# Kernel tuning notes

Measured on AMD Instinct MI355X. Metric: run time of the kernel, lower is better.

The kernel has to match this reference:

```python
import jax, jax.numpy as jnp
import numpy as np

H, HS, C = 16, 64, 1024  # num_heads, head_size, n_embd

def setup_inputs() -> dict:
    key = jax.random.key(0)
    ks = jax.random.split(key, 5)
    B, T = 2, 2048
    s = 1.0 / np.sqrt(C)
    return {
        "x": jax.random.normal(ks[0], (B, T, C), dtype=jnp.float32),
        "Wq": jax.random.normal(ks[1], (H, C, HS), dtype=jnp.float32) * s,
        "Wk": jax.random.normal(ks[2], (H, C, HS), dtype=jnp.float32) * s,
        "Wv": jax.random.normal(ks[3], (H, C, HS), dtype=jnp.float32) * s,
        "Wo": jax.random.normal(ks[4], (C, C), dtype=jnp.float32) * s,
    }

def reference(x, Wq, Wk, Wv, Wo):
    B, T, Cdim = x.shape
    scale = Cdim ** -0.5  # original scales by n_embd**-0.5, not head_size
    q = jnp.einsum('btc,hcd->bhtd', x, Wq)
    k = jnp.einsum('btc,hcd->bhtd', x, Wk)
    v = jnp.einsum('btc,hcd->bhtd', x, Wv)
    wei = jnp.einsum('bhtd,bhsd->bhts', q, k) * scale  # [B,H,T,T]
    causal = jnp.tril(jnp.ones((T, T), dtype=bool))
    wei = jnp.where(causal, wei, -jnp.inf)
    wei = jax.nn.softmax(wei, axis=-1)
    out = jnp.einsum('bhts,bhsd->bhtd', wei, v)  # [B,H,T,HS]
    out = out.transpose(0, 2, 1, 3).reshape(B, T, -1)  # concat heads -> [B,T,C]
    return out @ Wo.T
```

## Files before the change

kernel.cpp:

```cpp
#include <hip/hip_runtime.h>

typedef unsigned short ushort_t;
typedef __bf16 bf16x8 __attribute__((ext_vector_type(8)));
typedef float f32x4 __attribute__((ext_vector_type(4)));
typedef float f32x16 __attribute__((ext_vector_type(16)));
typedef unsigned short ushortx8 __attribute__((ext_vector_type(8)));
typedef unsigned int uintx4 __attribute__((ext_vector_type(4)));

#define NH 16
#define HS 64
#define CD 1024
#define NB 2
#define NT 2048
#define BT (NB * NT)
#define N3 (3 * CD)

#define L2E_DIV32 0.04508422002778011f

#define QKV_LD 2048
#define SLOT_BYTES 18432
#define WAVE_BYTES 4608
#define R0_SLOTS 796

__constant__ static const int QB_TAB[51] = {
  0,1,2, 3,3, 4,4, 5,5, 6,6,6, 7,7,7, 8,8,8,
  9,9,9,9, 10,10,10,10, 11,11,11,11,
  12,12,12,12,12, 13,13,13,13,13, 14,14,14,14,14,
  15,15,15,15,15,15};
__constant__ static const int K_TAB[51] = {
  1,1,1, 2,2, 2,2, 2,2, 3,3,3, 3,3,3, 3,3,3,
  4,4,4,4, 4,4,4,4, 4,4,4,4,
  5,5,5,5,5, 5,5,5,5,5, 5,5,5,5,5,
  6,6,6,6,6,6};
__constant__ static const int T0_TAB[51] = {
  0, 0, 0, 0,4, 0,5, 0,6, 0,5,10, 0,6,11, 0,6,12,
  0,5,10,15, 0,6,12,17, 0,6,12,18,
  0,6,11,16,21, 0,6,12,18,23, 0,6,12,18,24,
  0,6,12,17,22,27};
__constant__ static const int T1_TAB[51] = {
  2, 4, 6, 4,8, 5,10, 6,12, 5,10,14, 6,11,16, 6,12,18,
  5,10,15,20, 6,12,17,22, 6,12,18,24,
  6,11,16,21,26, 6,12,18,23,28, 6,12,18,24,30,
  6,12,17,22,27,32};
__constant__ static const int FIRSTC_TAB[16] = {
  0,1,2,3,5,7,9,12,15,18,22,26,30,35,40,45};


__device__ __forceinline__ ushort_t bf16_rne(float f) {
  union { float f; unsigned u; } v; v.f = f;
  unsigned u = v.u;
  unsigned r = (u + 0x7FFFu + ((u >> 16) & 1u)) >> 16;
  return (ushort_t)r;
}

__device__ __forceinline__ float bf2f(ushort_t u) {
  union { unsigned u; float f; } v; v.u = ((unsigned)u) << 16; return v.f;
}

__device__ __forceinline__ void gload_lds16(const ushort_t* g, ushort_t* l) {
  __builtin_amdgcn_global_load_lds(
      (const __attribute__((address_space(1))) unsigned int*)g,
      (__attribute__((address_space(3))) unsigned int*)l, 16, 0, 0);
}

__device__ __forceinline__ f32x4 mfma16(ushortx8 a, ushortx8 b, f32x4 c) {
  return __builtin_amdgcn_mfma_f32_16x16x32_bf16(
      __builtin_bit_cast(bf16x8, a), __builtin_bit_cast(bf16x8, b), c, 0, 0, 0);
}

__device__ __forceinline__ f32x16 mfma32(ushortx8 a, ushortx8 b, f32x16 c) {
  return __builtin_amdgcn_mfma_f32_32x32x16_bf16(
      __builtin_bit_cast(bf16x8, a), __builtin_bit_cast(bf16x8, b), c, 0, 0, 0);
}

__device__ __forceinline__ unsigned cvt_pk_bf16(float lo, float hi) {
  unsigned r;
  asm("v_cvt_pk_bf16_f32 %0, %1, %2" : "=v"(r) : "v"(lo), "v"(hi));
  return r;
}

__device__ __forceinline__ void plswap(unsigned &a, unsigned &b) {
  asm volatile("v_permlane32_swap_b32 %0, %1" : "+v"(a), "+v"(b));
}

__device__ __forceinline__ const char* slot_ptr(const char* wsb, const char* dout, int s) {
  return (s < R0_SLOTS) ? wsb + (size_t)s * SLOT_BYTES
                        : dout + (size_t)(s - R0_SLOTS) * SLOT_BYTES;
}


__global__ __launch_bounds__(256)
void pack_cast(const float4* __restrict__ in, ushort_t* __restrict__ out, int n4) {
  const int i = blockIdx.x * 256 + threadIdx.x;
  if (i >= n4) return;
  const float4 v = in[i];
  ushort4 r;
  r.x = bf16_rne(v.x); r.y = bf16_rne(v.y);
  r.z = bf16_rne(v.z); r.w = bf16_rne(v.w);
  *(ushort4*)(out + (size_t)i * 4) = r;
}

__global__ __launch_bounds__(256)
void pack_wqkv(const float* __restrict__ Wq, const float* __restrict__ Wk,
               const float* __restrict__ Wv, ushort_t* __restrict__ out) {
  __shared__ ushort_t tile[64 * 66];
  const int sh = blockIdx.y;
  const int s = sh >> 4, h = sh & 15;
  const float* W = (s == 0) ? Wq : ((s == 1) ? Wk : Wv);
  const int c0 = blockIdx.x * 64;
  const int t = threadIdx.x;
#pragma unroll
  for (int j = 0; j < 16; ++j) {
    const int idx = t + j * 256;
    const int ci = idx >> 6, d = idx & 63;
    const float v = W[(size_t)(h * 1024 + c0 + ci) * 64 + d];
    tile[d * 66 + ci] = bf16_rne(v);
  }
  __syncthreads();
#pragma unroll
  for (int j = 0; j < 16; ++j) {
    const int idx = t + j * 256;
    const int d = idx >> 6, ci = idx & 63;
    out[(size_t)(s * 1024 + h * 64 + d) * 1024 + c0 + ci] = tile[d * 66 + ci];
  }
}


template <int MODE>
__global__ __launch_bounds__(256)
void gemm_bt(const ushort_t* __restrict__ A, const ushort_t* __restrict__ Bt,
             void* __restrict__ Cv, ushort_t* __restrict__ Vt,
             int M, int N, int K) {
  __shared__ __align__(16) ushort_t ldsA[2][128 * 32];
  __shared__ __align__(16) ushort_t ldsB[2][128 * 32];
  const int tid = threadIdx.x;
  const int lane = tid & 63;
  const int wave = tid >> 6;
  const int row0 = blockIdx.y * 128;
  const int col0 = blockIdx.x * 128;
  const int wm = wave >> 1, wn = wave & 1;

  f32x4 acc[4][4] = {};

  const int ce = (tid & 3) * 8;

  auto stage = [&](int buf, int kt) {
    const int kbase = kt * 32;
#pragma unroll
    for (int j = 0; j < 2; ++j) {
      const int r = j * 64 + (tid >> 2);
      gload_lds16(A + (size_t)(row0 + r) * K + kbase + ce,
                  &ldsA[buf][(j * 256 + wave * 64) * 8]);
      gload_lds16(Bt + (size_t)(col0 + r) * K + kbase + ce,
                  &ldsB[buf][(j * 256 + wave * 64) * 8]);
    }
  };

  const int arow_off = (wm * 64 + (lane & 15)) * 32 + (lane >> 4) * 8;
  const int brow_off = (wn * 64 + (lane & 15)) * 32 + (lane >> 4) * 8;

  auto compute = [&](int buf) {
    ushortx8 af[4], bfr[4];
#pragma unroll
    for (int m = 0; m < 4; ++m)
      af[m] = *(const ushortx8*)&ldsA[buf][arow_off + m * 512];
#pragma unroll
    for (int n = 0; n < 4; ++n)
      bfr[n] = *(const ushortx8*)&ldsB[buf][brow_off + n * 512];
#pragma unroll
    for (int m = 0; m < 4; ++m)
#pragma unroll
      for (int n = 0; n < 4; ++n)
        acc[m][n] = mfma16(af[m], bfr[n], acc[m][n]);
  };

  stage(0, 0);
  __syncthreads();
  const int nk = K >> 5;
  for (int kt = 0; kt < nk; ++kt) {
    const int cur = kt & 1;
    if (kt + 1 < nk) stage(cur ^ 1, kt + 1);
    compute(cur);
    __syncthreads();
  }

#pragma unroll
  for (int m = 0; m < 4; ++m) {
    const int rbase = row0 + wm * 64 + m * 16 + (lane >> 4) * 4;
#pragma unroll
    for (int n = 0; n < 4; ++n) {
      const int col = col0 + wn * 64 + n * 16 + (lane & 15);
      if constexpr (MODE == 0) {
#pragma unroll
        for (int i = 0; i < 4; ++i)
          ((float*)Cv)[(size_t)(rbase + i) * N + col] = acc[m][n][i];
      } else {
        if (col < 2048) {
          const float sc = (col < 1024) ? L2E_DIV32 : 1.0f;
#pragma unroll
          for (int i = 0; i < 4; ++i)
            ((ushort_t*)Cv)[(size_t)(rbase + i) * QKV_LD + col] =
                bf16_rne(acc[m][n][i] * sc);
        } else {
          const int dcol = col - 2048;
          const int bI = rbase >> 11;
          const int t0i = rbase & 2047;
          ushort4 pk;
          pk.x = bf16_rne(acc[m][n][0]);
          pk.y = bf16_rne(acc[m][n][1]);
          pk.z = bf16_rne(acc[m][n][2]);
          pk.w = bf16_rne(acc[m][n][3]);
          *(ushort4*)(Vt + (size_t)(bI * 1024 + dcol) * NT + t0i) = pk;
        }
      }
    }
  }
}


__global__ __launch_bounds__(256, 4)
void attn_fwd9(const ushort_t* __restrict__ QKV, const ushort_t* __restrict__ Vt,
               ushort_t* __restrict__ O, char* __restrict__ wsb,
               char* __restrict__ dout) {
  __shared__ __align__(16) ushort_t KV[2][2][4096];

  const int tid = threadIdx.x;
  const int lane = tid & 63;
  const int w = tid >> 6;
  const int l31 = lane & 31;
  const int h = lane >> 5;

  const int x = blockIdx.x;
  const int bh = x & 31;
  const int c = 50 - (x >> 5);
  const int qb = QB_TAB[c];
  const int k  = K_TAB[c];
  const int t0 = T0_TAB[c];
  const int t1 = T1_TAB[c];
  const int nt = 2 * qb + 2;
  const bool lastc = (t1 == nt);

  const int b = bh >> 4, head = bh & 15;
  const size_t base = (size_t)b * NT * QKV_LD;
  const int qg = qb * 128 + w * 32 + l31;
  const int tmax = lastc ? (2 * qb + (w >> 1)) : (t1 - 1);

  int koff[4];
#pragma unroll
  for (int kc = 0; kc < 4; ++kc)
    koff[kc] = l31 * 128 + (((2 * kc + h) ^ (l31 & 7)) * 16);

  const int rowA = tid >> 3, ccA = tid & 7;
  const int rowB = 32 + rowA;
  const ushort_t* kg = QKV + base + 1024 + head * 64;
  const ushort_t* vg = Vt + (size_t)(bh * 64) * NT;
  const ushort_t* ksA = kg + (size_t)(t0 * 64 + rowA) * QKV_LD + ((ccA ^ (rowA & 7)) * 8);
  const ushort_t* ksB = kg + (size_t)(t0 * 64 + rowB) * QKV_LD + ((ccA ^ (rowB & 7)) * 8);
  const ushort_t* vsA = vg + (size_t)rowA * NT + t0 * 64 + ((ccA ^ (rowA & 7)) * 8);
  const ushort_t* vsB = vg + (size_t)rowB * NT + t0 * 64 + ((ccA ^ (rowB & 7)) * 8);
  const size_t kadv = (size_t)64 * QKV_LD;

  gload_lds16(ksA, &KV[0][0][w * 512]);
  gload_lds16(ksB, &KV[0][0][2048 + w * 512]);
  gload_lds16(vsA, &KV[0][1][w * 512]);
  gload_lds16(vsB, &KV[0][1][2048 + w * 512]);

  ushortx8 qf[4];
  {
    const ushort_t* qp = QKV + base + (size_t)qg * QKV_LD + head * 64 + h * 8;
#pragma unroll
    for (int kc = 0; kc < 4; ++kc) qf[kc] = *(const ushortx8*)(qp + kc * 16);
  }

  f32x16 oA = {}, oB = {};
  float m_r = -INFINITY, l_r = 0.f;

  auto half_pass = [&](f32x16 s, const char* vb, const int kc0, const bool msk) {
    if (msk) {
#pragma unroll
      for (int r = 0; r < 16; ++r) {
        const int krow = (r & 3) + 8 * (r >> 2) + 4 * h;
        if (krow > l31) s[r] = -INFINITY;
      }
    }
    float mm[8];
#pragma unroll
    for (int r = 0; r < 8; ++r) mm[r] = fmaxf(s[r], s[r + 8]);
#pragma unroll
    for (int st = 4; st >= 1; st >>= 1)
#pragma unroll
      for (int r = 0; r < st; ++r) mm[r] = fmaxf(mm[r], mm[r + st]);
    const float mx = fmaxf(mm[0], __shfl_xor(mm[0], 32, 64));
    if (__any(mx > m_r + 8.0f)) {
      const float mn = fmaxf(m_r, mx);
      const float al = exp2f(m_r - mn);
      m_r = mn; l_r *= al;
#pragma unroll
      for (int r = 0; r < 16; ++r) { oA[r] *= al; oB[r] *= al; }
    }
    unsigned u[8];
    float ps[4];
#pragma unroll
    for (int jj = 0; jj < 4; ++jj) ps[jj] = 0.f;
#pragma unroll
    for (int jj = 0; jj < 8; ++jj) {
      const float e0 = exp2f(s[2 * jj] - m_r);
      const float e1 = exp2f(s[2 * jj + 1] - m_r);
      u[jj] = cvt_pk_bf16(e0, e1);
      ps[jj & 3] += e0 + e1;
    }
    ps[0] += ps[2]; ps[1] += ps[3]; ps[0] += ps[1];
    l_r += ps[0] + __shfl_xor(ps[0], 32, 64);
    plswap(u[0], u[2]); plswap(u[1], u[3]);
    plswap(u[4], u[6]); plswap(u[5], u[7]);
#pragma unroll
    for (int q2 = 0; q2 < 2; ++q2) {
      uintx4 pw;
      pw[0] = u[4 * q2 + 0]; pw[1] = u[4 * q2 + 1];
      pw[2] = u[4 * q2 + 2]; pw[3] = u[4 * q2 + 3];
      const ushortx8 pav = __builtin_bit_cast(ushortx8, pw);
      oA = mfma32(*(const ushortx8*)(vb + koff[kc0 + q2]), pav, oA);
      oB = mfma32(*(const ushortx8*)(vb + 4096 + koff[kc0 + q2]), pav, oB);
    }
  };

  int curb = 0;
  for (int t = t0; t < t1; ++t) {
    const int nxt = curb ^ 1;
    if (t + 1 < t1) {
      ksA += kadv; ksB += kadv; vsA += 64; vsB += 64;
      gload_lds16(ksA, &KV[nxt][0][w * 512]);
      gload_lds16(ksB, &KV[nxt][0][2048 + w * 512]);
      gload_lds16(vsA, &KV[nxt][1][w * 512]);
      gload_lds16(vsB, &KV[nxt][1][2048 + w * 512]);
      asm volatile("s_waitcnt vmcnt(4)" ::: "memory");
    } else {
      asm volatile("s_waitcnt vmcnt(0)" ::: "memory");
    }
    __builtin_amdgcn_s_barrier();
    asm volatile("" ::: "memory");

    if (t <= tmax) {
      const bool diag = lastc && (t == tmax);
      const bool halfB = diag && ((w & 1) == 0);
      const char* kb = (const char*)&KV[curb][0][0];
      const char* vb = (const char*)&KV[curb][1][0];

      {
        f32x16 sA = {};
#pragma unroll
        for (int kc = 0; kc < 4; ++kc)
          sA = mfma32(*(const ushortx8*)(kb + koff[kc]), qf[kc], sA);
        half_pass(sA, vb, 0, diag && halfB);
      }
      if (!halfB) {
        f32x16 sB = {};
#pragma unroll
        for (int kc = 0; kc < 4; ++kc)
          sB = mfma32(*(const ushortx8*)(kb + 4096 + koff[kc]), qf[kc], sB);
        half_pass(sB, vb, 2, diag);
      }
    }

    __builtin_amdgcn_s_barrier();
    asm volatile("" ::: "memory");
    curb ^= 1;
  }

  if (k == 1) {
    const float inv_l = 1.0f / l_r;
    ushort_t* op = O + ((size_t)(b * NT + qg)) * 1024 + head * 64;
#pragma unroll
    for (int db = 0; db < 2; ++db)
#pragma unroll
      for (int g = 0; g < 4; ++g) {
        ushort4 pk;
        pk.x = bf16_rne((db ? oB[4 * g + 0] : oA[4 * g + 0]) * inv_l);
        pk.y = bf16_rne((db ? oB[4 * g + 1] : oA[4 * g + 1]) * inv_l);
        pk.z = bf16_rne((db ? oB[4 * g + 2] : oA[4 * g + 2]) * inv_l);
        pk.w = bf16_rne((db ? oB[4 * g + 3] : oA[4 * g + 3]) * inv_l);
        *(ushort4*)(op + db * 32 + 8 * g + 4 * h) = pk;
      }
  } else {
    const int s = bh * 51 + c;
    char* wb = (char*)slot_ptr(wsb, dout, s) + w * WAVE_BYTES;
#pragma unroll
    for (int g = 0; g < 4; ++g) {
      ushortx8 pk;
#pragma unroll
      for (int e2 = 0; e2 < 8; ++e2)
        pk[e2] = bf16_rne(g < 2 ? oA[g * 8 + e2] : oB[(g - 2) * 8 + e2]);
      *(ushortx8*)(wb + lane * 64 + g * 16) = pk;
    }
    *(float*)(wb + 4096 + lane * 4) = m_r;
    *(float*)(wb + 4352 + lane * 4) = l_r;
  }
}

__global__ __launch_bounds__(256)
void attn_merge(const char* __restrict__ wsb, const char* __restrict__ dout,
                ushort_t* __restrict__ O) {
  const int x = blockIdx.x;
  const int bh = x & 31;
  const int qb = 3 + (x >> 5);
  const int f = FIRSTC_TAB[qb];
  const int k = K_TAB[f];
  const int tid = threadIdx.x;
  const int lane = tid & 63;
  const int w = tid >> 6;
  const int l31 = lane & 31;
  const int h = lane >> 5;
  const int sbase = bh * 51 + f;

  float M = -INFINITY;
  for (int jj = 0; jj < k; ++jj) {
    const char* wb = slot_ptr(wsb, dout, sbase + jj) + w * WAVE_BYTES;
    M = fmaxf(M, *(const float*)(wb + 4096 + lane * 4));
  }
  float o[32];
#pragma unroll
  for (int r = 0; r < 32; ++r) o[r] = 0.f;
  float lacc = 0.f;
  for (int jj = 0; jj < k; ++jj) {
    const char* wb = slot_ptr(wsb, dout, sbase + jj) + w * WAVE_BYTES;
    const float a = exp2f(*(const float*)(wb + 4096 + lane * 4) - M);
    lacc += a * *(const float*)(wb + 4352 + lane * 4);
#pragma unroll
    for (int g = 0; g < 4; ++g) {
      const ushortx8 v = *(const ushortx8*)(wb + lane * 64 + g * 16);
#pragma unroll
      for (int e = 0; e < 8; ++e) o[g * 8 + e] += a * bf2f(v[e]);
    }
  }
  const float inv_l = 1.0f / lacc;
  const int b = bh >> 4, head = bh & 15;
  const int qg = qb * 128 + w * 32 + l31;
  ushort_t* op = O + ((size_t)(b * NT + qg)) * 1024 + head * 64;
#pragma unroll
  for (int db = 0; db < 2; ++db)
#pragma unroll
    for (int g = 0; g < 4; ++g) {
      ushort4 pk;
      pk.x = bf16_rne(o[db * 16 + 4 * g + 0] * inv_l);
      pk.y = bf16_rne(o[db * 16 + 4 * g + 1] * inv_l);
      pk.z = bf16_rne(o[db * 16 + 4 * g + 2] * inv_l);
      pk.w = bf16_rne(o[db * 16 + 4 * g + 3] * inv_l);
      *(ushort4*)(op + db * 32 + 8 * g + 4 * h) = pk;
    }
}


extern "C" void kernel_launch(void* const* d_in, const int* in_sizes, int n_in,
                              void* d_out, int out_size, void* d_ws, size_t ws_size,
                              hipStream_t stream) {
  (void)in_sizes; (void)n_in; (void)out_size; (void)ws_size;
  const float* x  = (const float*)d_in[0];
  const float* Wq = (const float*)d_in[1];
  const float* Wk = (const float*)d_in[2];
  const float* Wv = (const float*)d_in[3];
  const float* Wo = (const float*)d_in[4];

  char* ws = (char*)d_ws;
  ushort_t* Xbf    = (ushort_t*)(ws);
  ushort_t* Wqkv_t = (ushort_t*)(ws + 8388608);
  ushort_t* Wo_bf  = (ushort_t*)(ws + 14680064);
  ushort_t* QKV    = (ushort_t*)(ws + 16777216);
  ushort_t* Vt     = (ushort_t*)(ws + 33554432);
  ushort_t* Obf    = (ushort_t*)(ws + 41943040);

  pack_cast<<<4096, 256, 0, stream>>>((const float4*)x, Xbf, 1048576);
  pack_cast<<<1024, 256, 0, stream>>>((const float4*)Wo, Wo_bf, 262144);
  pack_wqkv<<<dim3(16, 48), 256, 0, stream>>>(Wq, Wk, Wv, Wqkv_t);

  gemm_bt<1><<<dim3(24, 32), 256, 0, stream>>>(Xbf, Wqkv_t, QKV, Vt, BT, N3, CD);
  attn_fwd9<<<1632, 256, 0, stream>>>(QKV, Vt, Obf, ws, (char*)d_out);
  attn_merge<<<416, 256, 0, stream>>>(ws, (char*)d_out, Obf);
  gemm_bt<0><<<dim3(8, 32), 256, 0, stream>>>(Obf, Wo_bf, d_out, nullptr, BT, CD, CD);
}
```

Before: 131.0 us.

## Repartition causal attention into 32 chunks per head and fuse cast kernels

Replaces the 51-chunk split-KV schedule per batch-head with a 32-chunk schedule. Each query block is split into 1-3 chunks of roughly equal KV-tile count, so the attention grid drops from 1632 to 1024 blocks and the merge grid from 416 to 352. A new lookup table maps each merged query block to its partial slots. It also fuses the two fp32-to-bf16 cast launches into one. The intent is to cut per-block overhead and the number of partial results to merge, at the risk of worse tail balance across CUs.

```diff
diff --git a/kernel.cpp b/kernel.cpp
--- a/kernel.cpp
+++ b/kernel.cpp
@@ -22,28 +22,21 @@
 #define WAVE_BYTES 4608
 #define R0_SLOTS 796
 
-__constant__ static const int QB_TAB[51] = {
-  0,1,2, 3,3, 4,4, 5,5, 6,6,6, 7,7,7, 8,8,8,
-  9,9,9,9, 10,10,10,10, 11,11,11,11,
-  12,12,12,12,12, 13,13,13,13,13, 14,14,14,14,14,
-  15,15,15,15,15,15};
-__constant__ static const int K_TAB[51] = {
-  1,1,1, 2,2, 2,2, 2,2, 3,3,3, 3,3,3, 3,3,3,
-  4,4,4,4, 4,4,4,4, 4,4,4,4,
-  5,5,5,5,5, 5,5,5,5,5, 5,5,5,5,5,
-  6,6,6,6,6,6};
-__constant__ static const int T0_TAB[51] = {
-  0, 0, 0, 0,4, 0,5, 0,6, 0,5,10, 0,6,11, 0,6,12,
-  0,5,10,15, 0,6,12,17, 0,6,12,18,
-  0,6,11,16,21, 0,6,12,18,23, 0,6,12,18,24,
-  0,6,12,17,22,27};
-__constant__ static const int T1_TAB[51] = {
-  2, 4, 6, 4,8, 5,10, 6,12, 5,10,14, 6,11,16, 6,12,18,
-  5,10,15,20, 6,12,17,22, 6,12,18,24,
-  6,11,16,21,26, 6,12,18,23,28, 6,12,18,24,30,
-  6,12,17,22,27,32};
-__constant__ static const int FIRSTC_TAB[16] = {
-  0,1,2,3,5,7,9,12,15,18,22,26,30,35,40,45};
+__constant__ static const int QB_TAB[32] = {
+  10,10,15,15, 4, 9, 9,13,14,14,14,15, 8, 8,12,12,
+  13,13, 3, 7, 7,11,11,11,12, 6, 6, 2, 5, 5, 1, 0};
+__constant__ static const int T0_TAB[32] = {
+   0,11, 0,11, 0, 0,10, 0, 0,10,20,22, 0, 9, 0, 9,
+  10,19, 0, 0, 8, 0, 8,16,18, 0, 7, 0, 0, 6, 0, 0};
+__constant__ static const int T1_TAB[32] = {
+  11,22,11,22,10,10,20,10,10,20,30,32, 9,18, 9,18,
+  19,28, 8, 8,16, 8,16,24,26, 7,14, 6, 6,12, 4, 2};
+__constant__ static const int K_TAB[32] = {
+   2, 2, 3, 3, 1, 2, 2, 3, 3, 3, 3, 3, 2, 2, 3, 3,
+   3, 3, 1, 2, 2, 3, 3, 3, 3, 2, 2, 1, 2, 2, 1, 1};
+__constant__ static const int MC_TAB[11][3] = {
+  {28,29, 0}, {25,26, 0}, {19,20, 0}, {12,13, 0}, { 5, 6, 0}, { 0, 1, 0},
+  {21,22,23}, {14,15,24}, { 7,16,17}, { 8, 9,10}, { 2, 3,11}};
 
 
 __device__ __forceinline__ ushort_t bf16_rne(float f) {
@@ -90,9 +83,12 @@
 
 
 __global__ __launch_bounds__(256)
-void pack_cast(const float4* __restrict__ in, ushort_t* __restrict__ out, int n4) {
-  const int i = blockIdx.x * 256 + threadIdx.x;
-  if (i >= n4) return;
+void pack_cast2(const float4* __restrict__ x, ushort_t* __restrict__ xout,
+                const float4* __restrict__ wo, ushort_t* __restrict__ woout) {
+  const int bid = blockIdx.x;
+  const float4* in = (bid < 4096) ? x : wo;
+  ushort_t* out = (bid < 4096) ? xout : woout;
+  const int i = ((bid < 4096) ? bid : (bid - 4096)) * 256 + threadIdx.x;
   const float4 v = in[i];
   ushort4 r;
   r.x = bf16_rne(v.x); r.y = bf16_rne(v.y);
@@ -219,9 +215,9 @@
 
 
 __global__ __launch_bounds__(256, 4)
-void attn_fwd9(const ushort_t* __restrict__ QKV, const ushort_t* __restrict__ Vt,
-               ushort_t* __restrict__ O, char* __restrict__ wsb,
-               char* __restrict__ dout) {
+void attn_fwd11(const ushort_t* __restrict__ QKV, const ushort_t* __restrict__ Vt,
+                ushort_t* __restrict__ O, char* __restrict__ wsb,
+                char* __restrict__ dout) {
   __shared__ __align__(16) ushort_t KV[2][2][4096];
 
   const int tid = threadIdx.x;
@@ -232,7 +228,7 @@
 
   const int x = blockIdx.x;
   const int bh = x & 31;
-  const int c = 50 - (x >> 5);
+  const int c = x >> 5;
   const int qb = QB_TAB[c];
   const int k  = K_TAB[c];
   const int t0 = T0_TAB[c];
@@ -382,7 +378,7 @@
         *(ushort4*)(op + db * 32 + 8 * g + 4 * h) = pk;
       }
   } else {
-    const int s = bh * 51 + c;
+    const int s = bh * 32 + c;
     char* wb = (char*)slot_ptr(wsb, dout, s) + w * WAVE_BYTES;
 #pragma unroll
     for (int g = 0; g < 4; ++g) {
@@ -402,19 +398,19 @@
                 ushort_t* __restrict__ O) {
   const int x = blockIdx.x;
   const int bh = x & 31;
-  const int qb = 3 + (x >> 5);
-  const int f = FIRSTC_TAB[qb];
-  const int k = K_TAB[f];
+  const int qi = x >> 5;
+  const int qb = 5 + qi;
+  const int k = (qb <= 10) ? 2 : 3;
   const int tid = threadIdx.x;
   const int lane = tid & 63;
   const int w = tid >> 6;
   const int l31 = lane & 31;
   const int h = lane >> 5;
-  const int sbase = bh * 51 + f;
 
   float M = -INFINITY;
   for (int jj = 0; jj < k; ++jj) {
-    const char* wb = slot_ptr(wsb, dout, sbase + jj) + w * WAVE_BYTES;
+    const int s = bh * 32 + MC_TAB[qi][jj];
+    const char* wb = slot_ptr(wsb, dout, s) + w * WAVE_BYTES;
     M = fmaxf(M, *(const float*)(wb + 4096 + lane * 4));
   }
   float o[32];
@@ -422,7 +418,8 @@
   for (int r = 0; r < 32; ++r) o[r] = 0.f;
   float lacc = 0.f;
   for (int jj = 0; jj < k; ++jj) {
-    const char* wb = slot_ptr(wsb, dout, sbase + jj) + w * WAVE_BYTES;
+    const int s = bh * 32 + MC_TAB[qi][jj];
+    const char* wb = slot_ptr(wsb, dout, s) + w * WAVE_BYTES;
     const float a = exp2f(*(const float*)(wb + 4096 + lane * 4) - M);
     lacc += a * *(const float*)(wb + 4352 + lane * 4);
 #pragma unroll
@@ -468,12 +465,11 @@
   ushort_t* Vt     = (ushort_t*)(ws + 33554432);
   ushort_t* Obf    = (ushort_t*)(ws + 41943040);
 
-  pack_cast<<<4096, 256, 0, stream>>>((const float4*)x, Xbf, 1048576);
-  pack_cast<<<1024, 256, 0, stream>>>((const float4*)Wo, Wo_bf, 262144);
+  pack_cast2<<<5120, 256, 0, stream>>>((const float4*)x, Xbf, (const float4*)Wo, Wo_bf);
   pack_wqkv<<<dim3(16, 48), 256, 0, stream>>>(Wq, Wk, Wv, Wqkv_t);
 
   gemm_bt<1><<<dim3(24, 32), 256, 0, stream>>>(Xbf, Wqkv_t, QKV, Vt, BT, N3, CD);
-  attn_fwd9<<<1632, 256, 0, stream>>>(QKV, Vt, Obf, ws, (char*)d_out);
-  attn_merge<<<416, 256, 0, stream>>>(ws, (char*)d_out, Obf);
+  attn_fwd11<<<1024, 256, 0, stream>>>(QKV, Vt, Obf, ws, (char*)d_out);
+  attn_merge<<<352, 256, 0, stream>>>(ws, (char*)d_out, Obf);
   gemm_bt<0><<<dim3(8, 32), 256, 0, stream>>>(Obf, Wo_bf, d_out, nullptr, BT, CD, CD);
 }
```

After: 122.8 us (median of 2 runs). 1.07x faster.
